# Optimization experiments

Measured on AMD Instinct MI355X. Metric: run time of the kernel, lower is better.

Reference implementation:

```python
import jax, jax.numpy as jnp
import numpy as np

N_NODES = 4096
N_GRAPHS = 512
NODES_PER_GRAPH = 8
N_EDGES = 32768
BN_EPS = 1e-5

lrelu = jax.nn.leaky_relu  # default negative_slope=0.01 matches F.leaky_relu


def lstm_seq(xs, W_ih, W_hh, b_ih, b_hh):
    """PyTorch-style single-layer LSTM over an unbatched sequence xs [T, In].
    Gate order i,f,g,o. Returns all hidden states [T, H]."""
    H = W_hh.shape[1]
    gx = xs @ W_ih.T + (b_ih + b_hh)  # [T, 4H] input projection hoisted out of scan

    def step(carry, g_t):
        h, c = carry
        g = g_t + h @ W_hh.T
        i, f, gg, o = jnp.split(g, 4)
        i = jax.nn.sigmoid(i)
        f = jax.nn.sigmoid(f)
        gg = jnp.tanh(gg)
        o = jax.nn.sigmoid(o)
        c = f * c + i * gg
        h = o * jnp.tanh(c)
        return (h, c), h

    init = (jnp.zeros((H,), xs.dtype), jnp.zeros((H,), xs.dtype))
    _, hs = jax.lax.scan(step, init, gx)
    return hs


def batch_norm(x, gamma, beta):
    # training-mode BatchNorm1d: batch stats over node dim, biased variance
    m = x.mean(axis=0)
    v = x.var(axis=0)
    return gamma * (x - m) / jnp.sqrt(v + BN_EPS) + beta


def gcn_conv(x, W, b, src, dst, edge_weight, num_nodes):
    # GCNConv(normalize=False): out_i = sum_{(s->t=i)} w_e * (x_s @ W^T) + b
    h = x @ W.T
    msg = edge_weight[:, None] * h[src]
    return jax.ops.segment_sum(msg, dst, num_segments=num_nodes) + b


def setup_inputs() -> dict:
    key = jax.random.key(0)
    ks = jax.random.split(key, 24)
    s = 0.02
    inp = {
        "x": jax.random.normal(ks[0], (N_NODES, 1280), jnp.float32),
        "edge_index": jax.random.randint(ks[1], (2, N_EDGES), 0, N_NODES, jnp.int32),
        "edge_weight": jax.random.uniform(ks[2], (N_EDGES,), jnp.float32),
        "batch": jnp.repeat(jnp.arange(N_GRAPHS, dtype=jnp.int32), NODES_PER_GRAPH),
        "W_ih1": s * jax.random.normal(ks[3], (2048, 1280), jnp.float32),
        "W_hh1": s * jax.random.normal(ks[4], (2048, 512), jnp.float32),
        "b_ih1": s * jax.random.normal(ks[5], (2048,), jnp.float32),
        "b_hh1": s * jax.random.normal(ks[6], (2048,), jnp.float32),
        "W_ih2": s * jax.random.normal(ks[7], (1024, 512), jnp.float32),
        "W_hh2": s * jax.random.normal(ks[8], (1024, 256), jnp.float32),
        "b_ih2": s * jax.random.normal(ks[9], (1024,), jnp.float32),
        "b_hh2": s * jax.random.normal(ks[10], (1024,), jnp.float32),
        "fc1_w": s * jax.random.normal(ks[11], (128, 256), jnp.float32),
        "fc1_b": s * jax.random.normal(ks[12], (128,), jnp.float32),
        "gcn1_w": s * jax.random.normal(ks[13], (64, 128), jnp.float32),
        "gcn1_b": s * jax.random.normal(ks[14], (64,), jnp.float32),
        "bn1_g": jnp.ones((64,), jnp.float32),
        "bn1_b": jnp.zeros((64,), jnp.float32),
        "gcn2_w": s * jax.random.normal(ks[15], (32, 64), jnp.float32),
        "gcn2_b": s * jax.random.normal(ks[16], (32,), jnp.float32),
        "bn2_g": jnp.ones((32,), jnp.float32),
        "bn2_b": jnp.zeros((32,), jnp.float32),
        "fc2_w": s * jax.random.normal(ks[17], (16, 32), jnp.float32),
        "fc2_b": s * jax.random.normal(ks[18], (16,), jnp.float32),
        "fc3_w": s * jax.random.normal(ks[19], (8, 16), jnp.float32),
        "fc3_b": s * jax.random.normal(ks[20], (8,), jnp.float32),
        "fc4_w": s * jax.random.normal(ks[21], (2, 8), jnp.float32),
        "fc4_b": s * jax.random.normal(ks[22], (2,), jnp.float32),
    }
    return inp


def reference(x, edge_index, edge_weight, batch,
              W_ih1, W_hh1, b_ih1, b_hh1,
              W_ih2, W_hh2, b_ih2, b_hh2,
              fc1_w, fc1_b,
              gcn1_w, gcn1_b, bn1_g, bn1_b,
              gcn2_w, gcn2_b, bn2_g, bn2_b,
              fc2_w, fc2_b, fc3_w, fc3_b, fc4_w, fc4_b):
    N = x.shape[0]
    src, dst = edge_index[0], edge_index[1]

    h = lrelu(lstm_seq(x, W_ih1, W_hh1, b_ih1, b_hh1))            # [N, 512]
    h = lrelu(lstm_seq(h, W_ih2, W_hh2, b_ih2, b_hh2))            # [N, 256]
    h = lrelu(h @ fc1_w.T + fc1_b)                                 # [N, 128]
    h = lrelu(batch_norm(gcn_conv(h, gcn1_w, gcn1_b, src, dst, edge_weight, N), bn1_g, bn1_b))  # [N, 64]
    h = lrelu(batch_norm(gcn_conv(h, gcn2_w, gcn2_b, src, dst, edge_weight, N), bn2_g, bn2_b))  # [N, 32]
    pooled = jax.ops.segment_sum(h, batch, num_segments=N_GRAPHS)  # global_add_pool [G, 32]
    out = lrelu(pooled @ fc2_w.T + fc2_b)                          # [G, 16]
    out = lrelu(out @ fc3_w.T + fc3_b)                             # [G, 8]
    out = lrelu(out @ fc4_w.T + fc4_b)                             # [G, 2]
    return out
```

## Files before the change

kernel.cpp:

```cpp
#include <hip/hip_runtime.h>
#include <math.h>

#define AGENT __HIP_MEMORY_SCOPE_AGENT
typedef unsigned long long u64;

__device__ __forceinline__ float sigf(float x) { return 1.f / (1.f + __expf(-x)); }
__device__ __forceinline__ float lrelu(float x) { return x > 0.f ? x : 0.01f * x; }
__device__ __forceinline__ u64 aload64(const u64* p) {
    return __hip_atomic_load(p, __ATOMIC_RELAXED, AGENT);
}
__device__ __forceinline__ void astore64(u64* p, u64 v) {
    __hip_atomic_store(p, v, __ATOMIC_RELAXED, AGENT);
}

template <bool LRELU>
__global__ __launch_bounds__(256) void gemm_bias(
    const float* __restrict__ A, const float* __restrict__ B,
    const float* __restrict__ bias1, const float* __restrict__ bias2,
    float* __restrict__ C, int M, int N, int K)
{
    __shared__ float As[16][68];
    __shared__ float Bs[16][68];
    const int tid = threadIdx.x;
    const int m0 = blockIdx.y * 64, n0 = blockIdx.x * 64;
    const int tm = tid >> 4, tn = tid & 15;
    const int lr = tid >> 2;
    const int lk = (tid & 3) * 4;
    float acc[4][4] = {};
    for (int k0 = 0; k0 < K; k0 += 16) {
        float4 av = make_float4(0.f, 0.f, 0.f, 0.f);
        if (m0 + lr < M) av = *(const float4*)&A[(size_t)(m0 + lr) * K + k0 + lk];
        As[lk + 0][lr] = av.x; As[lk + 1][lr] = av.y;
        As[lk + 2][lr] = av.z; As[lk + 3][lr] = av.w;
        float4 bv = make_float4(0.f, 0.f, 0.f, 0.f);
        if (n0 + lr < N) bv = *(const float4*)&B[(size_t)(n0 + lr) * K + k0 + lk];
        Bs[lk + 0][lr] = bv.x; Bs[lk + 1][lr] = bv.y;
        Bs[lk + 2][lr] = bv.z; Bs[lk + 3][lr] = bv.w;
        __syncthreads();
#pragma unroll
        for (int kk = 0; kk < 16; kk++) {
            float a[4], b[4];
#pragma unroll
            for (int i = 0; i < 4; i++) a[i] = As[kk][tm * 4 + i];
#pragma unroll
            for (int j = 0; j < 4; j++) b[j] = Bs[kk][tn * 4 + j];
#pragma unroll
            for (int i = 0; i < 4; i++)
#pragma unroll
                for (int j = 0; j < 4; j++) acc[i][j] += a[i] * b[j];
        }
        __syncthreads();
    }
#pragma unroll
    for (int i = 0; i < 4; i++) {
#pragma unroll
        for (int j = 0; j < 4; j++) {
            int mm = m0 + tm * 4 + i, nn = n0 + tn * 4 + j;
            if (mm < M && nn < N) {
                float v = acc[i][j];
                if (bias1) v += bias1[nn];
                if (bias2) v += bias2[nn];
                if (LRELU) v = lrelu(v);
                C[(size_t)mm * N + nn] = v;
            }
        }
    }
}

__global__ __launch_bounds__(256) void lstm_pipe(
    const float* __restrict__ gx1, const float* __restrict__ Whh1,
    const float* __restrict__ Wih2, const float* __restrict__ Whh2,
    const float* __restrict__ bih2, const float* __restrict__ bhh2,
    u64* __restrict__ h1pub, u64* __restrict__ h2pub,
    float* __restrict__ h2seq)
{
    const int wg = blockIdx.x, tid = threadIdx.x;
    const int r = tid & 31, p = tid >> 5;
    __shared__ float xl[512];
    __shared__ float hl[256];
    __shared__ float part[8][32];

    if (wg < 64) {
        const int jb = wg * 8;
        const int grow = (r >> 3) * 512 + jb + (r & 7);
        float w[64];
#pragma unroll
        for (int q = 0; q < 64; q++) w[q] = Whh1[(size_t)grow * 512 + p * 64 + q];
        float cstate = 0.f;

        for (int t = 0; t < 4096; ++t) {
            float gxv = 0.f;
            if (tid < 32) gxv = gx1[(size_t)t * 2048 + (tid >> 3) * 512 + jb + (tid & 7)];
            if (t > 0) {
                const u64* base = h1pub + (size_t)(t - 1) * 512;
                const u64 want = (u64)t;
                u64 a = aload64(base + 2 * tid);
                u64 b = aload64(base + 2 * tid + 1);
                while ((a >> 32) != want || (b >> 32) != want) {
                    if ((a >> 32) != want) a = aload64(base + 2 * tid);
                    if ((b >> 32) != want) b = aload64(base + 2 * tid + 1);
                }
                xl[2 * tid]     = __uint_as_float((unsigned)a);
                xl[2 * tid + 1] = __uint_as_float((unsigned)b);
            } else {
                xl[2 * tid] = 0.f; xl[2 * tid + 1] = 0.f;
            }
            __syncthreads();
            float acc = 0.f;
#pragma unroll
            for (int q = 0; q < 64; q++) acc += w[q] * xl[p * 64 + q];
            part[p][r] = acc;
            __syncthreads();
            if (tid < 32) {
                float s = gxv;
#pragma unroll
                for (int pp = 0; pp < 8; pp++) s += part[pp][tid];
                const int g = tid >> 3;
                float act = (g == 2) ? tanhf(s) : sigf(s);
                const int e = tid & 7;
                float vi = __shfl(act, e, 64);
                float vf = __shfl(act, e + 8, 64);
                float vg = __shfl(act, e + 16, 64);
                float vo = __shfl(act, e + 24, 64);
                if (tid < 8) {
                    float c = vf * cstate + vi * vg;
                    cstate = c;
                    float h = vo * tanhf(c);
                    astore64(h1pub + (size_t)t * 512 + jb + tid,
                             ((u64)(t + 1) << 32) | (u64)__float_as_uint(h));
                }
            }
        }
    } else {
        const int k = wg - 64, jb = k * 8;
        const int grow = (r >> 3) * 256 + jb + (r & 7);
        float wi[64], wh[32];
#pragma unroll
        for (int q = 0; q < 64; q++) wi[q] = Wih2[(size_t)grow * 512 + p * 64 + q];
#pragma unroll
        for (int q = 0; q < 32; q++) wh[q] = Whh2[(size_t)grow * 256 + p * 32 + q];
        float bs = 0.f;
        if (tid < 32) {
            int row = (tid >> 3) * 256 + jb + (tid & 7);
            bs = bih2[row] + bhh2[row];
        }
        float cstate = 0.f;

        for (int t = 0; t < 4096; ++t) {
            {
                const u64* b1 = h1pub + (size_t)t * 512;
                const u64* b2 = h2pub + (size_t)(t - 1) * 256;
                const u64 want1 = (u64)(t + 1);
                const u64 want2 = (u64)t;
                u64 a = aload64(b1 + 2 * tid);
                u64 b = aload64(b1 + 2 * tid + 1);
                u64 c = (t > 0) ? aload64(b2 + tid) : (want2 << 32);
                while ((a >> 32) != want1 || (b >> 32) != want1 || (c >> 32) != want2) {
                    if ((a >> 32) != want1) a = aload64(b1 + 2 * tid);
                    if ((b >> 32) != want1) b = aload64(b1 + 2 * tid + 1);
                    if ((c >> 32) != want2) c = aload64(b2 + tid);
                }
                xl[2 * tid]     = lrelu(__uint_as_float((unsigned)a));
                xl[2 * tid + 1] = lrelu(__uint_as_float((unsigned)b));
                hl[tid] = (t > 0) ? __uint_as_float((unsigned)c) : 0.f;
            }
            __syncthreads();
            float acc = 0.f;
#pragma unroll
            for (int q = 0; q < 64; q++) acc += wi[q] * xl[p * 64 + q];
#pragma unroll
            for (int q = 0; q < 32; q++) acc += wh[q] * hl[p * 32 + q];
            part[p][r] = acc;
            __syncthreads();
            if (tid < 32) {
                float s = bs;
#pragma unroll
                for (int pp = 0; pp < 8; pp++) s += part[pp][tid];
                const int g = tid >> 3;
                float act = (g == 2) ? tanhf(s) : sigf(s);
                const int e = tid & 7;
                float vi = __shfl(act, e, 64);
                float vf = __shfl(act, e + 8, 64);
                float vg = __shfl(act, e + 16, 64);
                float vo = __shfl(act, e + 24, 64);
                if (tid < 8) {
                    float c = vf * cstate + vi * vg;
                    cstate = c;
                    float h = vo * tanhf(c);
                    astore64(h2pub + (size_t)t * 256 + jb + tid,
                             ((u64)(t + 1) << 32) | (u64)__float_as_uint(h));
                    h2seq[(size_t)t * 256 + jb + tid] = lrelu(h);
                }
            }
        }
    }
}

__global__ void gcn_scatter(const float* __restrict__ m, const int* __restrict__ ei,
                            const float* __restrict__ ew, float* __restrict__ y,
                            int shift, int nE)
{
    int idx = blockIdx.x * 256 + threadIdx.x;
    int e = idx >> shift;
    if (e >= nE) return;
    int C = 1 << shift;
    int ch = idx & (C - 1);
    int s = ei[e], d = ei[nE + e];
    atomicAdd(&y[(size_t)d * C + ch], ew[e] * m[(size_t)s * C + ch]);
}

__global__ __launch_bounds__(256) void bn_stats(
    const float* __restrict__ x, const float* __restrict__ gamma,
    const float* __restrict__ beta, float* __restrict__ scale,
    float* __restrict__ shift, int Nn, int C)
{
    int ch = blockIdx.x;
    float s = 0.f, s2 = 0.f;
    for (int n = threadIdx.x; n < Nn; n += 256) {
        float v = x[(size_t)n * C + ch];
        s += v; s2 += v * v;
    }
    __shared__ float rs[256], rq[256];
    rs[threadIdx.x] = s; rq[threadIdx.x] = s2;
    __syncthreads();
    for (int o = 128; o > 0; o >>= 1) {
        if (threadIdx.x < o) {
            rs[threadIdx.x] += rs[threadIdx.x + o];
            rq[threadIdx.x] += rq[threadIdx.x + o];
        }
        __syncthreads();
    }
    if (threadIdx.x == 0) {
        float mean = rs[0] / Nn;
        float var = rq[0] / Nn - mean * mean;
        float inv = rsqrtf(var + 1e-5f);
        float sc = gamma[ch] * inv;
        scale[ch] = sc;
        shift[ch] = beta[ch] - mean * sc;
    }
}

__global__ void bn_apply(const float* __restrict__ x, const float* __restrict__ scale,
                         const float* __restrict__ shift, float* __restrict__ z,
                         int mask, int total)
{
    int idx = blockIdx.x * 256 + threadIdx.x;
    if (idx >= total) return;
    int ch = idx & mask;
    z[idx] = lrelu(x[idx] * scale[ch] + shift[ch]);
}

__global__ void pool_kernel(const float* __restrict__ z, const int* __restrict__ batch,
                            float* __restrict__ pooled, int total)
{
    int idx = blockIdx.x * 256 + threadIdx.x;
    if (idx >= total) return;
    int n = idx >> 5, ch = idx & 31;
    atomicAdd(&pooled[(size_t)batch[n] * 32 + ch], z[idx]);
}

__global__ void mlp_kernel(const float* __restrict__ pooled,
                           const float* __restrict__ w2, const float* __restrict__ b2,
                           const float* __restrict__ w3, const float* __restrict__ b3,
                           const float* __restrict__ w4, const float* __restrict__ b4,
                           float* __restrict__ out)
{
    int g = blockIdx.x * 256 + threadIdx.x;
    if (g >= 512) return;
    float pbuf[32];
#pragma unroll
    for (int i = 0; i < 32; i++) pbuf[i] = pooled[g * 32 + i];
    float a[16];
#pragma unroll
    for (int j = 0; j < 16; j++) {
        float s = b2[j];
#pragma unroll
        for (int i = 0; i < 32; i++) s += w2[j * 32 + i] * pbuf[i];
        a[j] = lrelu(s);
    }
    float c8[8];
#pragma unroll
    for (int j = 0; j < 8; j++) {
        float s = b3[j];
#pragma unroll
        for (int i = 0; i < 16; i++) s += w3[j * 16 + i] * a[i];
        c8[j] = lrelu(s);
    }
#pragma unroll
    for (int j = 0; j < 2; j++) {
        float s = b4[j];
#pragma unroll
        for (int i = 0; i < 8; i++) s += w4[j * 8 + i] * c8[i];
        out[g * 2 + j] = lrelu(s);
    }
}

extern "C" void kernel_launch(void* const* d_in, const int* in_sizes, int n_in,
                              void* d_out, int out_size, void* d_ws, size_t ws_size,
                              hipStream_t stream)
{
    (void)in_sizes; (void)n_in; (void)out_size; (void)ws_size;
    const float* x      = (const float*)d_in[0];
    const int*   ei     = (const int*)d_in[1];
    const float* ew     = (const float*)d_in[2];
    const int*   batch  = (const int*)d_in[3];
    const float* W_ih1  = (const float*)d_in[4];
    const float* W_hh1  = (const float*)d_in[5];
    const float* b_ih1  = (const float*)d_in[6];
    const float* b_hh1  = (const float*)d_in[7];
    const float* W_ih2  = (const float*)d_in[8];
    const float* W_hh2  = (const float*)d_in[9];
    const float* b_ih2  = (const float*)d_in[10];
    const float* b_hh2  = (const float*)d_in[11];
    const float* fc1_w  = (const float*)d_in[12];
    const float* fc1_b  = (const float*)d_in[13];
    const float* gcn1_w = (const float*)d_in[14];
    const float* bn1_g  = (const float*)d_in[16];
    const float* bn1_b  = (const float*)d_in[17];
    const float* gcn2_w = (const float*)d_in[18];
    const float* bn2_g  = (const float*)d_in[20];
    const float* bn2_b  = (const float*)d_in[21];
    const float* fc2_w  = (const float*)d_in[22];
    const float* fc2_b  = (const float*)d_in[23];
    const float* fc3_w  = (const float*)d_in[24];
    const float* fc3_b  = (const float*)d_in[25];
    const float* fc4_w  = (const float*)d_in[26];
    const float* fc4_b  = (const float*)d_in[27];
    float* out = (float*)d_out;

    float* ws    = (float*)d_ws;
    float* gx1   = ws;
    u64*   h1pub = (u64*)(gx1 + (size_t)4096 * 2048);
    u64*   h2pub = h1pub + (size_t)4096 * 512;
    float* h2seq = (float*)(h2pub + (size_t)4096 * 256);
    float* scale1 = h2seq + (size_t)4096 * 256;
    float* shift1 = scale1 + 64;
    float* scale2 = shift1 + 64;
    float* shift2 = scale2 + 32;
    float* h3    = ws;
    float* m1    = h3 + (size_t)4096 * 128;
    float* y1    = m1 + (size_t)4096 * 64;
    float* m2    = y1 + (size_t)4096 * 64;
    float* y2    = m2 + (size_t)4096 * 32;
    float* pooled = y2 + (size_t)4096 * 32;

    dim3 b256(256);

    hipMemsetAsync(h1pub, 0, (size_t)4096 * 768 * sizeof(u64), stream);

    gemm_bias<false><<<dim3(2048 / 64, 4096 / 64), b256, 0, stream>>>(
        x, W_ih1, b_ih1, b_hh1, gx1, 4096, 2048, 1280);

    lstm_pipe<<<96, b256, 0, stream>>>(gx1, W_hh1, W_ih2, W_hh2, b_ih2, b_hh2,
                                       h1pub, h2pub, h2seq);

    gemm_bias<true><<<dim3(128 / 64, 4096 / 64), b256, 0, stream>>>(
        h2seq, fc1_w, fc1_b, nullptr, h3, 4096, 128, 256);

    gemm_bias<false><<<dim3(1, 4096 / 64), b256, 0, stream>>>(
        h3, gcn1_w, nullptr, nullptr, m1, 4096, 64, 128);
    hipMemsetAsync(y1, 0, (size_t)4096 * 64 * sizeof(float), stream);
    gcn_scatter<<<(32768 * 64) / 256, b256, 0, stream>>>(m1, ei, ew, y1, 6, 32768);
    bn_stats<<<64, b256, 0, stream>>>(y1, bn1_g, bn1_b, scale1, shift1, 4096, 64);
    bn_apply<<<(4096 * 64) / 256, b256, 0, stream>>>(y1, scale1, shift1, y1, 63, 4096 * 64);

    gemm_bias<false><<<dim3(1, 4096 / 64), b256, 0, stream>>>(
        y1, gcn2_w, nullptr, nullptr, m2, 4096, 32, 64);
    hipMemsetAsync(y2, 0, (size_t)4096 * 32 * sizeof(float), stream);
    gcn_scatter<<<(32768 * 32) / 256, b256, 0, stream>>>(m2, ei, ew, y2, 5, 32768);
    bn_stats<<<32, b256, 0, stream>>>(y2, bn2_g, bn2_b, scale2, shift2, 4096, 32);
    bn_apply<<<(4096 * 32) / 256, b256, 0, stream>>>(y2, scale2, shift2, y2, 31, 4096 * 32);

    hipMemsetAsync(pooled, 0, (size_t)512 * 32 * sizeof(float), stream);
    pool_kernel<<<(4096 * 32) / 256, b256, 0, stream>>>(y2, batch, pooled, 4096 * 32);
    mlp_kernel<<<2, b256, 0, stream>>>(pooled, fc2_w, fc2_b, fc3_w, fc3_b,
                                       fc4_w, fc4_b, out);
}
```

Before: 7.744 ms.

## Remap LSTM recurrence threads to two rows each with padded float4 LDS reads

Reworks the thread mapping in the persistent LSTM pipeline kernel. Each thread now computes two gate rows over a 32-wide K slice, reading the shared hidden vector with padded float4 loads to avoid LDS bank conflicts and reuse each loaded value twice. The spin-wait uses a wave-wide __all, the gx prefetch moves to the last wave into a double-buffered shared array, and tanhf is replaced by an exp-based fast tanh. These changes aim to shorten the per-timestep serial critical path. The cost is a 16-way partial-sum reduction instead of 8-way, and slightly different tanh numerics.

```diff
diff --git a/kernel.cpp b/kernel.cpp
--- a/kernel.cpp
+++ b/kernel.cpp
@@ -5,6 +5,7 @@
 typedef unsigned long long u64;
 
 __device__ __forceinline__ float sigf(float x) { return 1.f / (1.f + __expf(-x)); }
+__device__ __forceinline__ float tanh_fast(float x) { return 1.f - 2.f / (__expf(2.f * x) + 1.f); }
 __device__ __forceinline__ float lrelu(float x) { return x > 0.f ? x : 0.01f * x; }
 __device__ __forceinline__ u64 aload64(const u64* p) {
     return __hip_atomic_load(p, __ATOMIC_RELAXED, AGENT);
@@ -67,6 +68,9 @@
     }
 }
 
+#define XPAD(i) ((i) + 4 * ((i) >> 5))
+#define HPAD(i) ((i) + 4 * ((i) >> 4))
+
 __global__ __launch_bounds__(256) void lstm_pipe(
     const float* __restrict__ gx1, const float* __restrict__ Whh1,
     const float* __restrict__ Wih2, const float* __restrict__ Whh2,
@@ -75,48 +79,70 @@
     float* __restrict__ h2seq)
 {
     const int wg = blockIdx.x, tid = threadIdx.x;
-    const int r = tid & 31, p = tid >> 5;
-    __shared__ float xl[512];
-    __shared__ float hl[256];
-    __shared__ float part[8][32];
+    const int s = tid >> 4;
+    const int rp = tid & 15;
+    const int row0 = 2 * rp, row1 = row0 + 1;
+    __shared__ float xl[16 * 36];
+    __shared__ float hl[16 * 20];
+    __shared__ float partb[16 * 34];
+    __shared__ float gxl[2][32];
 
     if (wg < 64) {
         const int jb = wg * 8;
-        const int grow = (r >> 3) * 512 + jb + (r & 7);
-        float w[64];
-#pragma unroll
-        for (int q = 0; q < 64; q++) w[q] = Whh1[(size_t)grow * 512 + p * 64 + q];
+        const int g0 = (row0 >> 3) * 512 + jb + (row0 & 7);
+        const int g1 = (row1 >> 3) * 512 + jb + (row1 & 7);
+        float w0[32], w1[32];
+        {
+            const float* W0 = Whh1 + (size_t)g0 * 512 + 32 * s;
+            const float* W1 = Whh1 + (size_t)g1 * 512 + 32 * s;
+#pragma unroll
+            for (int q = 0; q < 8; q++) {
+                float4 a = *(const float4*)&W0[4 * q];
+                float4 b = *(const float4*)&W1[4 * q];
+                w0[4 * q] = a.x; w0[4 * q + 1] = a.y; w0[4 * q + 2] = a.z; w0[4 * q + 3] = a.w;
+                w1[4 * q] = b.x; w1[4 * q + 1] = b.y; w1[4 * q + 2] = b.z; w1[4 * q + 3] = b.w;
+            }
+        }
         float cstate = 0.f;
 
         for (int t = 0; t < 4096; ++t) {
             float gxv = 0.f;
-            if (tid < 32) gxv = gx1[(size_t)t * 2048 + (tid >> 3) * 512 + jb + (tid & 7)];
+            if (tid >= 224) {
+                int gi = tid - 224;
+                gxv = gx1[(size_t)t * 2048 + (gi >> 3) * 512 + jb + (gi & 7)];
+            }
+            float fa = 0.f, fb = 0.f;
             if (t > 0) {
                 const u64* base = h1pub + (size_t)(t - 1) * 512;
                 const u64 want = (u64)t;
                 u64 a = aload64(base + 2 * tid);
                 u64 b = aload64(base + 2 * tid + 1);
-                while ((a >> 32) != want || (b >> 32) != want) {
+                while (!__all(((a >> 32) == want) & ((b >> 32) == want))) {
                     if ((a >> 32) != want) a = aload64(base + 2 * tid);
                     if ((b >> 32) != want) b = aload64(base + 2 * tid + 1);
                 }
-                xl[2 * tid]     = __uint_as_float((unsigned)a);
-                xl[2 * tid + 1] = __uint_as_float((unsigned)b);
-            } else {
-                xl[2 * tid] = 0.f; xl[2 * tid + 1] = 0.f;
-            }
+                fa = __uint_as_float((unsigned)a);
+                fb = __uint_as_float((unsigned)b);
+            }
+            if (tid >= 224) gxl[t & 1][tid - 224] = gxv;
+            *(float2*)&xl[XPAD(2 * tid)] = make_float2(fa, fb);
             __syncthreads();
-            float acc = 0.f;
-#pragma unroll
-            for (int q = 0; q < 64; q++) acc += w[q] * xl[p * 64 + q];
-            part[p][r] = acc;
+            float acc0 = 0.f, acc1 = 0.f;
+#pragma unroll
+            for (int q4 = 0; q4 < 8; ++q4) {
+                float4 xv = *(const float4*)&xl[36 * s + 4 * q4];
+                acc0 += w0[4 * q4] * xv.x + w0[4 * q4 + 1] * xv.y
+                      + w0[4 * q4 + 2] * xv.z + w0[4 * q4 + 3] * xv.w;
+                acc1 += w1[4 * q4] * xv.x + w1[4 * q4 + 1] * xv.y
+                      + w1[4 * q4 + 2] * xv.z + w1[4 * q4 + 3] * xv.w;
+            }
+            *(float2*)&partb[s * 34 + 2 * rp] = make_float2(acc0, acc1);
             __syncthreads();
             if (tid < 32) {
-                float s = gxv;
-#pragma unroll
-                for (int pp = 0; pp < 8; pp++) s += part[pp][tid];
-                const int g = tid >> 3;
-                float act = (g == 2) ? tanhf(s) : sigf(s);
+                float sum = gxl[t & 1][tid];
+#pragma unroll
+                for (int ss = 0; ss < 16; ++ss) sum += partb[ss * 34 + tid];
+                float act = ((tid >> 3) == 2) ? tanh_fast(sum) : sigf(sum);
                 const int e = tid & 7;
                 float vi = __shfl(act, e, 64);
                 float vf = __shfl(act, e + 8, 64);
@@ -125,7 +151,7 @@
                 if (tid < 8) {
                     float c = vf * cstate + vi * vg;
                     cstate = c;
-                    float h = vo * tanhf(c);
+                    float h = vo * tanh_fast(c);
                     astore64(h1pub + (size_t)t * 512 + jb + tid,
                              ((u64)(t + 1) << 32) | (u64)__float_as_uint(h));
                 }
@@ -133,12 +159,29 @@
         }
     } else {
         const int k = wg - 64, jb = k * 8;
-        const int grow = (r >> 3) * 256 + jb + (r & 7);
-        float wi[64], wh[32];
-#pragma unroll
-        for (int q = 0; q < 64; q++) wi[q] = Wih2[(size_t)grow * 512 + p * 64 + q];
-#pragma unroll
-        for (int q = 0; q < 32; q++) wh[q] = Whh2[(size_t)grow * 256 + p * 32 + q];
+        const int g0 = (row0 >> 3) * 256 + jb + (row0 & 7);
+        const int g1 = (row1 >> 3) * 256 + jb + (row1 & 7);
+        float wx0[32], wx1[32], wh0[16], wh1[16];
+        {
+            const float* X0 = Wih2 + (size_t)g0 * 512 + 32 * s;
+            const float* X1 = Wih2 + (size_t)g1 * 512 + 32 * s;
+#pragma unroll
+            for (int q = 0; q < 8; q++) {
+                float4 a = *(const float4*)&X0[4 * q];
+                float4 b = *(const float4*)&X1[4 * q];
+                wx0[4 * q] = a.x; wx0[4 * q + 1] = a.y; wx0[4 * q + 2] = a.z; wx0[4 * q + 3] = a.w;
+                wx1[4 * q] = b.x; wx1[4 * q + 1] = b.y; wx1[4 * q + 2] = b.z; wx1[4 * q + 3] = b.w;
+            }
+            const float* H0 = Whh2 + (size_t)g0 * 256 + 16 * s;
+            const float* H1 = Whh2 + (size_t)g1 * 256 + 16 * s;
+#pragma unroll
+            for (int q = 0; q < 4; q++) {
+                float4 a = *(const float4*)&H0[4 * q];
+                float4 b = *(const float4*)&H1[4 * q];
+                wh0[4 * q] = a.x; wh0[4 * q + 1] = a.y; wh0[4 * q + 2] = a.z; wh0[4 * q + 3] = a.w;
+                wh1[4 * q] = b.x; wh1[4 * q + 1] = b.y; wh1[4 * q + 2] = b.z; wh1[4 * q + 3] = b.w;
+            }
+        }
         float bs = 0.f;
         if (tid < 32) {
             int row = (tid >> 3) * 256 + jb + (tid & 7);
@@ -155,29 +198,42 @@
                 u64 a = aload64(b1 + 2 * tid);
                 u64 b = aload64(b1 + 2 * tid + 1);
                 u64 c = (t > 0) ? aload64(b2 + tid) : (want2 << 32);
-                while ((a >> 32) != want1 || (b >> 32) != want1 || (c >> 32) != want2) {
+                while (!__all(((a >> 32) == want1) & ((b >> 32) == want1) &
+                              ((c >> 32) == want2))) {
                     if ((a >> 32) != want1) a = aload64(b1 + 2 * tid);
                     if ((b >> 32) != want1) b = aload64(b1 + 2 * tid + 1);
                     if ((c >> 32) != want2) c = aload64(b2 + tid);
                 }
-                xl[2 * tid]     = lrelu(__uint_as_float((unsigned)a));
-                xl[2 * tid + 1] = lrelu(__uint_as_float((unsigned)b));
-                hl[tid] = (t > 0) ? __uint_as_float((unsigned)c) : 0.f;
+                *(float2*)&xl[XPAD(2 * tid)] =
+                    make_float2(lrelu(__uint_as_float((unsigned)a)),
+                                lrelu(__uint_as_float((unsigned)b)));
+                hl[HPAD(tid)] = (t > 0) ? __uint_as_float((unsigned)c) : 0.f;
             }
             __syncthreads();
-            float acc = 0.f;
-#pragma unroll
-            for (int q = 0; q < 64; q++) acc += wi[q] * xl[p * 64 + q];
-#pragma unroll
-            for (int q = 0; q < 32; q++) acc += wh[q] * hl[p * 32 + q];
-            part[p][r] = acc;
+            float acc0 = 0.f, acc1 = 0.f;
+#pragma unroll
+            for (int q4 = 0; q4 < 8; ++q4) {
+                float4 xv = *(const float4*)&xl[36 * s + 4 * q4];
+                acc0 += wx0[4 * q4] * xv.x + wx0[4 * q4 + 1] * xv.y
+                      + wx0[4 * q4 + 2] * xv.z + wx0[4 * q4 + 3] * xv.w;
+                acc1 += wx1[4 * q4] * xv.x + wx1[4 * q4 + 1] * xv.y
+                      + wx1[4 * q4 + 2] * xv.z + wx1[4 * q4 + 3] * xv.w;
+            }
+#pragma unroll
+            for (int q4 = 0; q4 < 4; ++q4) {
+                float4 hv = *(const float4*)&hl[20 * s + 4 * q4];
+                acc0 += wh0[4 * q4] * hv.x + wh0[4 * q4 + 1] * hv.y
+                      + wh0[4 * q4 + 2] * hv.z + wh0[4 * q4 + 3] * hv.w;
+                acc1 += wh1[4 * q4] * hv.x + wh1[4 * q4 + 1] * hv.y
+                      + wh1[4 * q4 + 2] * hv.z + wh1[4 * q4 + 3] * hv.w;
+            }
+            *(float2*)&partb[s * 34 + 2 * rp] = make_float2(acc0, acc1);
             __syncthreads();
             if (tid < 32) {
-                float s = bs;
-#pragma unroll
-                for (int pp = 0; pp < 8; pp++) s += part[pp][tid];
-                const int g = tid >> 3;
-                float act = (g == 2) ? tanhf(s) : sigf(s);
+                float sum = bs;
+#pragma unroll
+                for (int ss = 0; ss < 16; ++ss) sum += partb[ss * 34 + tid];
+                float act = ((tid >> 3) == 2) ? tanh_fast(sum) : sigf(sum);
                 const int e = tid & 7;
                 float vi = __shfl(act, e, 64);
                 float vf = __shfl(act, e + 8, 64);
@@ -186,7 +242,7 @@
                 if (tid < 8) {
                     float c = vf * cstate + vi * vg;
                     cstate = c;
-                    float h = vo * tanhf(c);
+                    float h = vo * tanh_fast(c);
                     astore64(h2pub + (size_t)t * 256 + jb + tid,
                              ((u64)(t + 1) << 32) | (u64)__float_as_uint(h));
                     h2seq[(size_t)t * 256 + jb + tid] = lrelu(h);
```

Result: slower. 8.079 ms (+4.3%).

## Merge LSTM1 and LSTM2 work into every workgroup with skewed timesteps

Applied to the files above, without the earlier changes.

The two-layer LSTM pipeline used 64 workgroups for layer 1 and 32 for layer 2. It now runs 64 workgroups, each computing 8 layer-1 units at step t and 4 layer-2 units at step t-1, with one combined wait and fewer barriers per step. The wait uses a wave-wide __all poll instead of per-lane retry loops. tanhf is replaced by an exp-based fast tanh. Each workgroup now carries more registers and serial work per step, and the fast tanh slightly changes numerics.

```diff
diff --git a/kernel.cpp b/kernel.cpp
--- a/kernel.cpp
+++ b/kernel.cpp
@@ -5,6 +5,7 @@
 typedef unsigned long long u64;
 
 __device__ __forceinline__ float sigf(float x) { return 1.f / (1.f + __expf(-x)); }
+__device__ __forceinline__ float tanh_fast(float x) { return 1.f - 2.f / (__expf(2.f * x) + 1.f); }
 __device__ __forceinline__ float lrelu(float x) { return x > 0.f ? x : 0.01f * x; }
 __device__ __forceinline__ u64 aload64(const u64* p) {
     return __hip_atomic_load(p, __ATOMIC_RELAXED, AGENT);
@@ -75,122 +76,132 @@
     float* __restrict__ h2seq)
 {
     const int wg = blockIdx.x, tid = threadIdx.x;
-    const int r = tid & 31, p = tid >> 5;
+    const int p = tid >> 5, r = tid & 31;
+    const int jb1 = wg * 8, jb2 = wg * 4;
     __shared__ float xl[512];
-    __shared__ float hl[256];
-    __shared__ float part[8][32];
-
-    if (wg < 64) {
-        const int jb = wg * 8;
-        const int grow = (r >> 3) * 512 + jb + (r & 7);
-        float w[64];
-#pragma unroll
-        for (int q = 0; q < 64; q++) w[q] = Whh1[(size_t)grow * 512 + p * 64 + q];
-        float cstate = 0.f;
-
-        for (int t = 0; t < 4096; ++t) {
-            float gxv = 0.f;
-            if (tid < 32) gxv = gx1[(size_t)t * 2048 + (tid >> 3) * 512 + jb + (tid & 7)];
-            if (t > 0) {
-                const u64* base = h1pub + (size_t)(t - 1) * 512;
-                const u64 want = (u64)t;
-                u64 a = aload64(base + 2 * tid);
-                u64 b = aload64(base + 2 * tid + 1);
-                while ((a >> 32) != want || (b >> 32) != want) {
-                    if ((a >> 32) != want) a = aload64(base + 2 * tid);
-                    if ((b >> 32) != want) b = aload64(base + 2 * tid + 1);
-                }
-                xl[2 * tid]     = __uint_as_float((unsigned)a);
-                xl[2 * tid + 1] = __uint_as_float((unsigned)b);
+    __shared__ float cat[768];
+    __shared__ float part1[8][33];
+    __shared__ float part2[16][17];
+
+    const int grow1 = (r >> 3) * 512 + jb1 + (r & 7);
+    float w1[64];
+#pragma unroll
+    for (int q = 0; q < 64; q++) w1[q] = Whh1[(size_t)grow1 * 512 + p * 64 + q];
+
+    const int row2 = r & 15, seg2 = (p << 1) | (r >> 4);
+    const int grow2 = (row2 >> 2) * 256 + jb2 + (row2 & 3);
+    float w2r[48];
+#pragma unroll
+    for (int j = 0; j < 48; j++) {
+        int idx = seg2 * 48 + j;
+        w2r[j] = (idx < 512) ? Wih2[(size_t)grow2 * 512 + idx]
+                             : Whh2[(size_t)grow2 * 256 + (idx - 512)];
+    }
+
+    float bs = 0.f;
+    if (tid >= 32 && tid < 48) {
+        int l = tid - 32;
+        int row = (l >> 2) * 256 + jb2 + (l & 3);
+        bs = bih2[row] + bhh2[row];
+    }
+    float c1 = 0.f, c2 = 0.f;
+
+    for (int t = 0; t <= 4096; ++t) {
+        float gxv = 0.f;
+        if (t < 4096 && tid < 32)
+            gxv = gx1[(size_t)t * 2048 + (tid >> 3) * 512 + jb1 + (tid & 7)];
+
+        unsigned va = 0, vb = 0, vc = 0;
+        if (t >= 1) {
+            const u64* p1 = h1pub + (size_t)(t - 1) * 512 + 2 * tid;
+            const unsigned want = (unsigned)t;
+            if (t >= 2) {
+                const u64* p2 = h2pub + (size_t)(t - 2) * 256 + tid;
+                u64 a, b, c;
+                do {
+                    a = aload64(p1); b = aload64(p1 + 1); c = aload64(p2);
+                } while (!__all(((unsigned)(a >> 32) == want) &
+                                ((unsigned)(b >> 32) == want) &
+                                ((unsigned)(c >> 32) == want)));
+                va = (unsigned)a; vb = (unsigned)b; vc = (unsigned)c;
             } else {
-                xl[2 * tid] = 0.f; xl[2 * tid + 1] = 0.f;
-            }
-            __syncthreads();
-            float acc = 0.f;
-#pragma unroll
-            for (int q = 0; q < 64; q++) acc += w[q] * xl[p * 64 + q];
-            part[p][r] = acc;
-            __syncthreads();
+                u64 a, b;
+                do {
+                    a = aload64(p1); b = aload64(p1 + 1);
+                } while (!__all(((unsigned)(a >> 32) == want) &
+                                ((unsigned)(b >> 32) == want)));
+                va = (unsigned)a; vb = (unsigned)b;
+            }
+        }
+        {
+            float fa = __uint_as_float(va), fb = __uint_as_float(vb);
+            xl[2 * tid] = fa;
+            xl[2 * tid + 1] = fb;
+            cat[2 * tid] = lrelu(fa);
+            cat[2 * tid + 1] = lrelu(fb);
+            cat[512 + tid] = __uint_as_float(vc);
+        }
+        __syncthreads();
+
+        {
+            float a0 = 0.f, a1 = 0.f, a2 = 0.f, a3 = 0.f;
+            const float* xs = &xl[p * 64];
+#pragma unroll
+            for (int q = 0; q < 16; q++) {
+                a0 += w1[4 * q + 0] * xs[4 * q + 0];
+                a1 += w1[4 * q + 1] * xs[4 * q + 1];
+                a2 += w1[4 * q + 2] * xs[4 * q + 2];
+                a3 += w1[4 * q + 3] * xs[4 * q + 3];
+            }
+            part1[p][r] = (a0 + a1) + (a2 + a3);
+        }
+        {
+            float b0 = 0.f, b1 = 0.f, b2 = 0.f, b3 = 0.f;
+            const float* cs = &cat[seg2 * 48];
+#pragma unroll
+            for (int j = 0; j < 12; j++) {
+                b0 += w2r[4 * j + 0] * cs[4 * j + 0];
+                b1 += w2r[4 * j + 1] * cs[4 * j + 1];
+                b2 += w2r[4 * j + 2] * cs[4 * j + 2];
+                b3 += w2r[4 * j + 3] * cs[4 * j + 3];
+            }
+            part2[seg2][row2] = (b0 + b1) + (b2 + b3);
+        }
+        __syncthreads();
+
+        if (tid < 64) {
+            float act = 0.f;
             if (tid < 32) {
                 float s = gxv;
 #pragma unroll
-                for (int pp = 0; pp < 8; pp++) s += part[pp][tid];
-                const int g = tid >> 3;
-                float act = (g == 2) ? tanhf(s) : sigf(s);
-                const int e = tid & 7;
-                float vi = __shfl(act, e, 64);
-                float vf = __shfl(act, e + 8, 64);
-                float vg = __shfl(act, e + 16, 64);
-                float vo = __shfl(act, e + 24, 64);
-                if (tid < 8) {
-                    float c = vf * cstate + vi * vg;
-                    cstate = c;
-                    float h = vo * tanhf(c);
-                    astore64(h1pub + (size_t)t * 512 + jb + tid,
-                             ((u64)(t + 1) << 32) | (u64)__float_as_uint(h));
-                }
-            }
-        }
-    } else {
-        const int k = wg - 64, jb = k * 8;
-        const int grow = (r >> 3) * 256 + jb + (r & 7);
-        float wi[64], wh[32];
-#pragma unroll
-        for (int q = 0; q < 64; q++) wi[q] = Wih2[(size_t)grow * 512 + p * 64 + q];
-#pragma unroll
-        for (int q = 0; q < 32; q++) wh[q] = Whh2[(size_t)grow * 256 + p * 32 + q];
-        float bs = 0.f;
-        if (tid < 32) {
-            int row = (tid >> 3) * 256 + jb + (tid & 7);
-            bs = bih2[row] + bhh2[row];
-        }
-        float cstate = 0.f;
-
-        for (int t = 0; t < 4096; ++t) {
-            {
-                const u64* b1 = h1pub + (size_t)t * 512;
-                const u64* b2 = h2pub + (size_t)(t - 1) * 256;
-                const u64 want1 = (u64)(t + 1);
-                const u64 want2 = (u64)t;
-                u64 a = aload64(b1 + 2 * tid);
-                u64 b = aload64(b1 + 2 * tid + 1);
-                u64 c = (t > 0) ? aload64(b2 + tid) : (want2 << 32);
-                while ((a >> 32) != want1 || (b >> 32) != want1 || (c >> 32) != want2) {
-                    if ((a >> 32) != want1) a = aload64(b1 + 2 * tid);
-                    if ((b >> 32) != want1) b = aload64(b1 + 2 * tid + 1);
-                    if ((c >> 32) != want2) c = aload64(b2 + tid);
-                }
-                xl[2 * tid]     = lrelu(__uint_as_float((unsigned)a));
-                xl[2 * tid + 1] = lrelu(__uint_as_float((unsigned)b));
-                hl[tid] = (t > 0) ? __uint_as_float((unsigned)c) : 0.f;
-            }
-            __syncthreads();
-            float acc = 0.f;
-#pragma unroll
-            for (int q = 0; q < 64; q++) acc += wi[q] * xl[p * 64 + q];
-#pragma unroll
-            for (int q = 0; q < 32; q++) acc += wh[q] * hl[p * 32 + q];
-            part[p][r] = acc;
-            __syncthreads();
-            if (tid < 32) {
+                for (int pp = 0; pp < 8; pp++) s += part1[pp][tid];
+                act = ((tid >> 3) == 2) ? tanh_fast(s) : sigf(s);
+            } else if (tid < 48) {
                 float s = bs;
 #pragma unroll
-                for (int pp = 0; pp < 8; pp++) s += part[pp][tid];
-                const int g = tid >> 3;
-                float act = (g == 2) ? tanhf(s) : sigf(s);
-                const int e = tid & 7;
-                float vi = __shfl(act, e, 64);
-                float vf = __shfl(act, e + 8, 64);
-                float vg = __shfl(act, e + 16, 64);
-                float vo = __shfl(act, e + 24, 64);
-                if (tid < 8) {
-                    float c = vf * cstate + vi * vg;
-                    cstate = c;
-                    float h = vo * tanhf(c);
-                    astore64(h2pub + (size_t)t * 256 + jb + tid,
-                             ((u64)(t + 1) << 32) | (u64)__float_as_uint(h));
-                    h2seq[(size_t)t * 256 + jb + tid] = lrelu(h);
-                }
+                for (int ss = 0; ss < 16; ss++) s += part2[ss][tid - 32];
+                act = (((tid - 32) >> 2) == 2) ? tanh_fast(s) : sigf(s);
+            }
+            const int base = tid & 32;
+            const int gsz = base ? 4 : 8;
+            const int e = tid & 7;
+            float vi = __shfl(act, base + e, 64);
+            float vf = __shfl(act, base + gsz + e, 64);
+            float vg = __shfl(act, base + 2 * gsz + e, 64);
+            float vo = __shfl(act, base + 3 * gsz + e, 64);
+            if (tid < 8 && t < 4096) {
+                c1 = vf * c1 + vi * vg;
+                float h = vo * tanh_fast(c1);
+                astore64(h1pub + (size_t)t * 512 + jb1 + tid,
+                         ((u64)(t + 1) << 32) | (u64)__float_as_uint(h));
+            }
+            if (tid >= 32 && tid < 36 && t >= 1) {
+                c2 = vf * c2 + vi * vg;
+                float h = vo * tanh_fast(c2);
+                const size_t ofs = (size_t)(t - 1) * 256 + jb2 + (tid - 32);
+                astore64(h2pub + ofs,
+                         ((u64)(t + 1) << 32) | (u64)__float_as_uint(h));
+                h2seq[ofs] = lrelu(h);
             }
         }
     }
@@ -328,30 +339,31 @@
     const float* fc4_b  = (const float*)d_in[27];
     float* out = (float*)d_out;
 
-    float* ws    = (float*)d_ws;
-    float* gx1   = ws;
-    u64*   h1pub = (u64*)(gx1 + (size_t)4096 * 2048);
-    u64*   h2pub = h1pub + (size_t)4096 * 512;
-    float* h2seq = (float*)(h2pub + (size_t)4096 * 256);
-    float* scale1 = h2seq + (size_t)4096 * 256;
+    char* base = (char*)d_ws;
+    const size_t MB = 1024 * 1024;
+    float* gx1    = (float*)base;
+    u64*   h1pub  = (u64*)(base + 32 * MB);
+    u64*   h2pub  = (u64*)(base + 48 * MB);
+    float* h2seq  = (float*)(base + 56 * MB);
+    float* scale1 = (float*)(base + 60 * MB);
     float* shift1 = scale1 + 64;
     float* scale2 = shift1 + 64;
     float* shift2 = scale2 + 32;
-    float* h3    = ws;
-    float* m1    = h3 + (size_t)4096 * 128;
-    float* y1    = m1 + (size_t)4096 * 64;
-    float* m2    = y1 + (size_t)4096 * 64;
-    float* y2    = m2 + (size_t)4096 * 32;
+    float* h3     = (float*)base;
+    float* m1     = h3 + (size_t)4096 * 128;
+    float* y1     = m1 + (size_t)4096 * 64;
+    float* m2     = y1 + (size_t)4096 * 64;
+    float* y2     = m2 + (size_t)4096 * 32;
     float* pooled = y2 + (size_t)4096 * 32;
 
     dim3 b256(256);
 
-    hipMemsetAsync(h1pub, 0, (size_t)4096 * 768 * sizeof(u64), stream);
+    hipMemsetAsync(h1pub, 0, (size_t)24 * MB, stream);
 
     gemm_bias<false><<<dim3(2048 / 64, 4096 / 64), b256, 0, stream>>>(
         x, W_ih1, b_ih1, b_hh1, gx1, 4096, 2048, 1280);
 
-    lstm_pipe<<<96, b256, 0, stream>>>(gx1, W_hh1, W_ih2, W_hh2, b_ih2, b_hh2,
+    lstm_pipe<<<64, b256, 0, stream>>>(gx1, W_hh1, W_ih2, W_hh2, b_ih2, b_hh2,
                                        h1pub, h2pub, h2seq);
 
     gemm_bias<true><<<dim3(128 / 64, 4096 / 64), b256, 0, stream>>>(
```

Result: slower. 12.33 ms (+59.2%).

## Restructure LSTM pipeline with dedicated poll waves and local hidden-state reuse

Applied to the files above, without the earlier changes.

The persistent LSTM kernel is restructured so that wave 0 computes the gates and writes its own new hidden values straight into shared memory. Waves 1-3 meanwhile poll the other workgroups' published values for the next step, with a wave-wide __all exit and double-buffered loads. This drops one __syncthreads per step and takes the global-memory polling off the gate-computation path. It also prefetches gx, splits the dot-product accumulators four ways, and uses an exp-based tanh, which risks small accuracy differences.

```diff
diff --git a/kernel.cpp b/kernel.cpp
--- a/kernel.cpp
+++ b/kernel.cpp
@@ -5,6 +5,7 @@
 typedef unsigned long long u64;
 
 __device__ __forceinline__ float sigf(float x) { return 1.f / (1.f + __expf(-x)); }
+__device__ __forceinline__ float tanh_fast(float x) { return 1.f - 2.f / (__expf(2.f * x) + 1.f); }
 __device__ __forceinline__ float lrelu(float x) { return x > 0.f ? x : 0.01f * x; }
 __device__ __forceinline__ u64 aload64(const u64* p) {
     return __hip_atomic_load(p, __ATOMIC_RELAXED, AGENT);
@@ -75,7 +76,9 @@
     float* __restrict__ h2seq)
 {
     const int wg = blockIdx.x, tid = threadIdx.x;
-    const int r = tid & 31, p = tid >> 5;
+    const int wv = tid >> 6;
+    const int i192 = tid - 64;
+    const int p = tid >> 5, r = tid & 31;
     __shared__ float xl[512];
     __shared__ float hl[256];
     __shared__ float part[8][32];
@@ -86,54 +89,82 @@
         float w[64];
 #pragma unroll
         for (int q = 0; q < 64; q++) w[q] = Whh1[(size_t)grow * 512 + p * 64 + q];
-        float cstate = 0.f;
+        float c1 = 0.f, gxv = 0.f;
+
+        int we[3]; bool rl[3];
+        if (wv > 0) {
+#pragma unroll
+            for (int j = 0; j < 3; j++) {
+                int wd = i192 + 192 * j;
+                bool real = (wd < 512) && !(wd >= jb && wd < jb + 8);
+                rl[j] = real; we[j] = real ? wd : 0;
+            }
+        }
+        xl[2 * tid] = 0.f; xl[2 * tid + 1] = 0.f;
+        if (tid < 32) gxv = gx1[(size_t)(tid >> 3) * 512 + jb + (tid & 7)];
+        __syncthreads();
 
         for (int t = 0; t < 4096; ++t) {
-            float gxv = 0.f;
-            if (tid < 32) gxv = gx1[(size_t)t * 2048 + (tid >> 3) * 512 + jb + (tid & 7)];
-            if (t > 0) {
-                const u64* base = h1pub + (size_t)(t - 1) * 512;
-                const u64 want = (u64)t;
-                u64 a = aload64(base + 2 * tid);
-                u64 b = aload64(base + 2 * tid + 1);
-                while ((a >> 32) != want || (b >> 32) != want) {
-                    if ((a >> 32) != want) a = aload64(base + 2 * tid);
-                    if ((b >> 32) != want) b = aload64(base + 2 * tid + 1);
+            float a0 = 0.f, a1 = 0.f, a2 = 0.f, a3 = 0.f;
+            const float* xs = &xl[p * 64];
+#pragma unroll
+            for (int q = 0; q < 16; q++) {
+                a0 += w[4 * q + 0] * xs[4 * q + 0];
+                a1 += w[4 * q + 1] * xs[4 * q + 1];
+                a2 += w[4 * q + 2] * xs[4 * q + 2];
+                a3 += w[4 * q + 3] * xs[4 * q + 3];
+            }
+            part[p][r] = (a0 + a1) + (a2 + a3);
+            __syncthreads();
+            if (wv == 0) {
+                if (tid < 32) {
+                    float s = gxv;
+#pragma unroll
+                    for (int pp = 0; pp < 8; pp++) s += part[pp][tid];
+                    float act = ((tid >> 3) == 2) ? tanh_fast(s) : sigf(s);
+                    const int e = tid & 7;
+                    float vi = __shfl(act, e, 64);
+                    float vf = __shfl(act, e + 8, 64);
+                    float vg = __shfl(act, e + 16, 64);
+                    float vo = __shfl(act, e + 24, 64);
+                    if (tid < 8) {
+                        c1 = vf * c1 + vi * vg;
+                        float h = vo * tanh_fast(c1);
+                        astore64(h1pub + (size_t)t * 512 + jb + tid,
+                                 ((u64)(t + 1) << 32) | (u64)__float_as_uint(h));
+                        xl[jb + tid] = h;
+                    }
+                    if (t + 1 < 4096)
+                        gxv = gx1[(size_t)(t + 1) * 2048 + (tid >> 3) * 512 + jb + (tid & 7)];
                 }
-                xl[2 * tid]     = __uint_as_float((unsigned)a);
-                xl[2 * tid + 1] = __uint_as_float((unsigned)b);
-            } else {
-                xl[2 * tid] = 0.f; xl[2 * tid + 1] = 0.f;
+            } else if (t + 1 < 4096) {
+                const u64* bp = h1pub + (size_t)t * 512;
+                const unsigned want = (unsigned)(t + 1);
+                u64 v0[3], v1[3];
+#pragma unroll
+                for (int j = 0; j < 3; j++) v0[j] = aload64(bp + we[j]);
+#pragma unroll
+                for (int j = 0; j < 3; j++) v1[j] = aload64(bp + we[j]);
+                for (;;) {
+                    bool ok = true;
+#pragma unroll
+                    for (int j = 0; j < 3; j++)
+                        ok &= (!rl[j]) || ((unsigned)(v0[j] >> 32) == want);
+                    if (__all(ok)) break;
+#pragma unroll
+                    for (int j = 0; j < 3; j++) v0[j] = v1[j];
+#pragma unroll
+                    for (int j = 0; j < 3; j++) v1[j] = aload64(bp + we[j]);
+                }
+#pragma unroll
+                for (int j = 0; j < 3; j++)
+                    if (rl[j]) xl[we[j]] = __uint_as_float((unsigned)v0[j]);
             }
             __syncthreads();
-            float acc = 0.f;
-#pragma unroll
-            for (int q = 0; q < 64; q++) acc += w[q] * xl[p * 64 + q];
-            part[p][r] = acc;
-            __syncthreads();
-            if (tid < 32) {
-                float s = gxv;
-#pragma unroll
-                for (int pp = 0; pp < 8; pp++) s += part[pp][tid];
-                const int g = tid >> 3;
-                float act = (g == 2) ? tanhf(s) : sigf(s);
-                const int e = tid & 7;
-                float vi = __shfl(act, e, 64);
-                float vf = __shfl(act, e + 8, 64);
-                float vg = __shfl(act, e + 16, 64);
-                float vo = __shfl(act, e + 24, 64);
-                if (tid < 8) {
-                    float c = vf * cstate + vi * vg;
-                    cstate = c;
-                    float h = vo * tanhf(c);
-                    astore64(h1pub + (size_t)t * 512 + jb + tid,
-                             ((u64)(t + 1) << 32) | (u64)__float_as_uint(h));
-                }
-            }
         }
     } else {
-        const int k = wg - 64, jb = k * 8;
-        const int grow = (r >> 3) * 256 + jb + (r & 7);
+        const int k = wg - 64, jb2 = k * 8;
+        const int grow = (r >> 3) * 256 + jb2 + (r & 7);
         float wi[64], wh[32];
 #pragma unroll
         for (int q = 0; q < 64; q++) wi[q] = Wih2[(size_t)grow * 512 + p * 64 + q];
@@ -141,57 +172,124 @@
         for (int q = 0; q < 32; q++) wh[q] = Whh2[(size_t)grow * 256 + p * 32 + q];
         float bs = 0.f;
         if (tid < 32) {
-            int row = (tid >> 3) * 256 + jb + (tid & 7);
+            int row = (tid >> 3) * 256 + jb2 + (tid & 7);
             bs = bih2[row] + bhh2[row];
         }
-        float cstate = 0.f;
+        float c2 = 0.f;
+
+        int we[4]; bool rl[4], ish1[4];
+        if (wv > 0) {
+#pragma unroll
+            for (int j = 0; j < 4; j++) {
+                int wd = i192 + 192 * j;
+                bool h1w = (wd < 512);
+                bool real = h1w || !((wd - 512) >= jb2 && (wd - 512) < jb2 + 8);
+                ish1[j] = h1w; rl[j] = real; we[j] = wd;
+            }
+        }
+        hl[tid] = 0.f;
+        if (wv > 0) {
+            const u64* bp = h1pub;
+            const unsigned want = 1u;
+            u64 v0[4], v1[4];
+#pragma unroll
+            for (int j = 0; j < 4; j++) v0[j] = aload64(bp + (ish1[j] ? we[j] : 0));
+#pragma unroll
+            for (int j = 0; j < 4; j++) v1[j] = aload64(bp + (ish1[j] ? we[j] : 0));
+            for (;;) {
+                bool ok = true;
+#pragma unroll
+                for (int j = 0; j < 4; j++)
+                    ok &= (!ish1[j]) || ((unsigned)(v0[j] >> 32) == want);
+                if (__all(ok)) break;
+#pragma unroll
+                for (int j = 0; j < 4; j++) v0[j] = v1[j];
+#pragma unroll
+                for (int j = 0; j < 4; j++) v1[j] = aload64(bp + (ish1[j] ? we[j] : 0));
+            }
+#pragma unroll
+            for (int j = 0; j < 4; j++)
+                if (ish1[j]) xl[we[j]] = lrelu(__uint_as_float((unsigned)v0[j]));
+        }
+        __syncthreads();
 
         for (int t = 0; t < 4096; ++t) {
-            {
-                const u64* b1 = h1pub + (size_t)t * 512;
-                const u64* b2 = h2pub + (size_t)(t - 1) * 256;
-                const u64 want1 = (u64)(t + 1);
-                const u64 want2 = (u64)t;
-                u64 a = aload64(b1 + 2 * tid);
-                u64 b = aload64(b1 + 2 * tid + 1);
-                u64 c = (t > 0) ? aload64(b2 + tid) : (want2 << 32);
-                while ((a >> 32) != want1 || (b >> 32) != want1 || (c >> 32) != want2) {
-                    if ((a >> 32) != want1) a = aload64(b1 + 2 * tid);
-                    if ((b >> 32) != want1) b = aload64(b1 + 2 * tid + 1);
-                    if ((c >> 32) != want2) c = aload64(b2 + tid);
+            float a0 = 0.f, a1 = 0.f, a2 = 0.f, a3 = 0.f;
+            const float* xs = &xl[p * 64];
+            const float* hs = &hl[p * 32];
+#pragma unroll
+            for (int q = 0; q < 16; q++) {
+                a0 += wi[4 * q + 0] * xs[4 * q + 0];
+                a1 += wi[4 * q + 1] * xs[4 * q + 1];
+                a2 += wi[4 * q + 2] * xs[4 * q + 2];
+                a3 += wi[4 * q + 3] * xs[4 * q + 3];
+            }
+#pragma unroll
+            for (int q = 0; q < 8; q++) {
+                a0 += wh[4 * q + 0] * hs[4 * q + 0];
+                a1 += wh[4 * q + 1] * hs[4 * q + 1];
+                a2 += wh[4 * q + 2] * hs[4 * q + 2];
+                a3 += wh[4 * q + 3] * hs[4 * q + 3];
+            }
+            part[p][r] = (a0 + a1) + (a2 + a3);
+            __syncthreads();
+            if (wv == 0) {
+                if (tid < 32) {
+                    float s = bs;
+#pragma unroll
+                    for (int pp = 0; pp < 8; pp++) s += part[pp][tid];
+                    float act = ((tid >> 3) == 2) ? tanh_fast(s) : sigf(s);
+                    const int e = tid & 7;
+                    float vi = __shfl(act, e, 64);
+                    float vf = __shfl(act, e + 8, 64);
+                    float vg = __shfl(act, e + 16, 64);
+                    float vo = __shfl(act, e + 24, 64);
+                    if (tid < 8) {
+                        c2 = vf * c2 + vi * vg;
+                        float h = vo * tanh_fast(c2);
+                        const size_t ofs = (size_t)t * 256 + jb2 + tid;
+                        astore64(h2pub + ofs,
+                                 ((u64)(t + 1) << 32) | (u64)__float_as_uint(h));
+                        h2seq[ofs] = lrelu(h);
+                        hl[jb2 + tid] = h;
+                    }
                 }
-                xl[2 * tid]     = lrelu(__uint_as_float((unsigned)a));
-                xl[2 * tid + 1] = lrelu(__uint_as_float((unsigned)b));
-                hl[tid] = (t > 0) ? __uint_as_float((unsigned)c) : 0.f;
+            } else if (t + 1 < 4096) {
+                const u64* bp1 = h1pub + (size_t)(t + 1) * 512;
+                const u64* bp2 = h2pub + (size_t)t * 256;
+                const unsigned w1 = (unsigned)(t + 2), w2 = (unsigned)(t + 1);
+                const u64* ad[4];
+#pragma unroll
+                for (int j = 0; j < 4; j++)
+                    ad[j] = ish1[j] ? (bp1 + we[j])
+                                    : (bp2 + (rl[j] ? (we[j] - 512) : 0));
+                u64 v0[4], v1[4];
+#pragma unroll
+                for (int j = 0; j < 4; j++) v0[j] = aload64(ad[j]);
+#pragma unroll
+                for (int j = 0; j < 4; j++) v1[j] = aload64(ad[j]);
+                for (;;) {
+                    bool ok = true;
+#pragma unroll
+                    for (int j = 0; j < 4; j++) {
+                        unsigned want = ish1[j] ? w1 : w2;
+                        ok &= (!rl[j]) || ((unsigned)(v0[j] >> 32) == want);
+                    }
+                    if (__all(ok)) break;
+#pragma unroll
+                    for (int j = 0; j < 4; j++) v0[j] = v1[j];
+#pragma unroll
+                    for (int j = 0; j < 4; j++) v1[j] = aload64(ad[j]);
+                }
+#pragma unroll
+                for (int j = 0; j < 4; j++) {
+                    if (!rl[j]) continue;
+                    float f = __uint_as_float((unsigned)v0[j]);
+                    if (ish1[j]) xl[we[j]] = lrelu(f);
+                    else hl[we[j] - 512] = f;
+                }
             }
             __syncthreads();
-            float acc = 0.f;
-#pragma unroll
-            for (int q = 0; q < 64; q++) acc += wi[q] * xl[p * 64 + q];
-#pragma unroll
-            for (int q = 0; q < 32; q++) acc += wh[q] * hl[p * 32 + q];
-            part[p][r] = acc;
-            __syncthreads();
-            if (tid < 32) {
-                float s = bs;
-#pragma unroll
-                for (int pp = 0; pp < 8; pp++) s += part[pp][tid];
-                const int g = tid >> 3;
-                float act = (g == 2) ? tanhf(s) : sigf(s);
-                const int e = tid & 7;
-                float vi = __shfl(act, e, 64);
-                float vf = __shfl(act, e + 8, 64);
-                float vg = __shfl(act, e + 16, 64);
-                float vo = __shfl(act, e + 24, 64);
-                if (tid < 8) {
-                    float c = vf * cstate + vi * vg;
-                    cstate = c;
-                    float h = vo * tanhf(c);
-                    astore64(h2pub + (size_t)t * 256 + jb + tid,
-                             ((u64)(t + 1) << 32) | (u64)__float_as_uint(h));
-                    h2seq[(size_t)t * 256 + jb + tid] = lrelu(h);
-                }
-            }
         }
     }
 }
@@ -328,25 +426,26 @@
     const float* fc4_b  = (const float*)d_in[27];
     float* out = (float*)d_out;
 
-    float* ws    = (float*)d_ws;
-    float* gx1   = ws;
-    u64*   h1pub = (u64*)(gx1 + (size_t)4096 * 2048);
-    u64*   h2pub = h1pub + (size_t)4096 * 512;
-    float* h2seq = (float*)(h2pub + (size_t)4096 * 256);
-    float* scale1 = h2seq + (size_t)4096 * 256;
+    char* base = (char*)d_ws;
+    const size_t MB = 1024 * 1024;
+    float* gx1    = (float*)base;
+    u64*   h1pub  = (u64*)(base + 32 * MB);
+    u64*   h2pub  = (u64*)(base + 48 * MB);
+    float* h2seq  = (float*)(base + 56 * MB);
+    float* scale1 = (float*)(base + 60 * MB);
     float* shift1 = scale1 + 64;
     float* scale2 = shift1 + 64;
     float* shift2 = scale2 + 32;
-    float* h3    = ws;
-    float* m1    = h3 + (size_t)4096 * 128;
-    float* y1    = m1 + (size_t)4096 * 64;
-    float* m2    = y1 + (size_t)4096 * 64;
-    float* y2    = m2 + (size_t)4096 * 32;
+    float* h3     = (float*)base;
+    float* m1     = h3 + (size_t)4096 * 128;
+    float* y1     = m1 + (size_t)4096 * 64;
+    float* m2     = y1 + (size_t)4096 * 64;
+    float* y2     = m2 + (size_t)4096 * 32;
     float* pooled = y2 + (size_t)4096 * 32;
 
     dim3 b256(256);
 
-    hipMemsetAsync(h1pub, 0, (size_t)4096 * 768 * sizeof(u64), stream);
+    hipMemsetAsync(h1pub, 0, (size_t)24 * MB, stream);
 
     gemm_bias<false><<<dim3(2048 / 64, 4096 / 64), b256, 0, stream>>>(
         x, W_ih1, b_ih1, b_hh1, gx1, 4096, 2048, 1280);
```

Result: slower. 9.699 ms (+25.2%).
